# Optimization experiments

Measured on AMD Instinct MI355X. Metric: run time of the kernel, lower is better.

The kernel has to match this reference:

```python
import jax, jax.numpy as jnp
import numpy as np
from jax import lax

WIN = 9  # NCC window per axis (default [9]*3)

# 3x3x3 edge/shape kernels, shape [O=1, I=1, 3, 3, 3]
_LAP = np.zeros((3, 3, 3), np.float32)
_LAP[1, 1, 1] = 6.0
_LAP[0, 1, 1] = _LAP[2, 1, 1] = -1.0
_LAP[1, 0, 1] = _LAP[1, 2, 1] = -1.0
_LAP[1, 1, 0] = _LAP[1, 1, 2] = -1.0
LAP_K = jnp.asarray(_LAP)[None, None]

_row = np.array([[-1.0, 0.0, 1.0], [-2.0, 0.0, 2.0], [-1.0, 0.0, 1.0]], np.float32)
SOBEL_X = jnp.asarray(np.stack([_row, _row, _row], axis=0))[None, None]
_plane = np.array([[-1.0, -2.0, -1.0], [-1.0, -2.0, -1.0], [-1.0, -2.0, -1.0]], np.float32)
SOBEL_Y = jnp.asarray(np.stack([_plane, np.zeros((3, 3), np.float32), -_plane], axis=0))[None, None]
_zp = np.array([[-1.0, -1.0, -1.0], [0.0, 0.0, 0.0], [1.0, 1.0, 1.0]], np.float32)
SOBEL_Z = jnp.asarray(np.stack([_zp, 2.0 * _zp, _zp], axis=0))[None, None]


def conv3d(x, k, pad):
    # x: [N,C,D,H,W], k: [O,I,kd,kh,kw]
    return lax.conv_general_dilated(x, k, (1, 1, 1), [(pad, pad)] * 3)


def box_sum(x, win=WIN):
    # Separable all-ones box filter == dense ones conv (same math, fewer FLOPs)
    pad = win // 2
    for axis in range(3):
        kshape = [1, 1, 1, 1, 1]
        kshape[2 + axis] = win
        k = jnp.ones(kshape, x.dtype)
        padding = [(pad, pad) if a == axis else (0, 0) for a in range(3)]
        x = lax.conv_general_dilated(x, k, (1, 1, 1), padding)
    return x


def ncc_vxm(Ii, Ji, win=WIN):
    win_size = float(win ** 3)
    I2, J2, IJ = Ii * Ii, Ji * Ji, Ii * Ji
    I_sum = box_sum(Ii, win)
    J_sum = box_sum(Ji, win)
    I2_sum = box_sum(I2, win)
    J2_sum = box_sum(J2, win)
    IJ_sum = box_sum(IJ, win)
    u_I = I_sum / win_size
    u_J = J_sum / win_size
    cross = IJ_sum - u_J * I_sum - u_I * J_sum + u_I * u_J * win_size
    I_var = I2_sum - 2.0 * u_I * I_sum + u_I * u_I * win_size
    J_var = J2_sum - 2.0 * u_J * J_sum + u_J * u_J * win_size
    cc = cross * cross / (I_var * J_var + 1e-5)
    return -jnp.mean(cc)


def edge_detection(v):
    return conv3d(v, LAP_K, pad=1)


def shape_detection(v):
    gx = conv3d(v, SOBEL_X, pad=1)
    gy = conv3d(v, SOBEL_Y, pad=1)
    gz = conv3d(v, SOBEL_Z, pad=1)
    return jnp.sqrt(gx * gx + gy * gy + gz * gz)


def setup_inputs() -> dict:
    key = jax.random.key(0)
    k1, k2 = jax.random.split(key)
    shape = (1, 1, 160, 192, 160)
    y_true = jax.random.uniform(k1, shape, dtype=jnp.float32)
    y_pred = jax.random.uniform(k2, shape, dtype=jnp.float32)
    return {"y_true": y_true, "y_pred": y_pred}


def reference(y_true, y_pred):
    loss_orig = ncc_vxm(y_true, y_pred)
    loss_edge = ncc_vxm(edge_detection(y_true), edge_detection(y_pred))
    loss_shape = ncc_vxm(shape_detection(y_true), shape_detection(y_pred))
    return 0.8 * loss_orig + 0.1 * loss_edge + 0.1 * loss_shape
```

## Files before the change

kernel.cpp:

```cpp
#include <hip/hip_runtime.h>
#include <hip/hip_fp16.h>
#include <math.h>

#define DD 160
#define HHH 192
#define WWW 160
constexpr int HW = HHH * WWW;
constexpr int NV = DD * HHH * WWW;
constexpr int W4 = WWW / 4;
constexpr int HC = 4;
constexpr int DC = 4;
constexpr int SC = 8;

constexpr int NB_WH  = (W4 * DD * (HHH / HC)) / 256;
constexpr int NB_SO  = (W4 * HHH * (DD / SC)) / 256;
constexpr int NB_LAP = (NV / 4) / 256;
constexpr int NB_DCC = (W4 * HHH * (DD / DC)) / 256;

__device__ __forceinline__ int xcd_swz(int b, int n) {
    int q = n >> 3;
    return (b & 7) * q + (b >> 3);
}

__device__ __forceinline__ float4 ldg4(const float* __restrict__ p, int idx, bool ok) {
    float4 z = make_float4(0.f, 0.f, 0.f, 0.f);
    return ok ? *(const float4*)(p + idx) : z;
}

__device__ __forceinline__ void st_h4(__half* __restrict__ t, int idx,
                                      float s0, float s1, float s2, float s3) {
    union { __half2 h2[2]; uint2 u; } pk;
    pk.h2[0] = __floats2half2_rn(s0, s1);
    pk.h2[1] = __floats2half2_rn(s2, s3);
    *(uint2*)(t + idx) = pk.u;
}

__device__ __forceinline__ void ld_h4(const __half* __restrict__ t, int idx, float o[4]) {
    union { __half2 h2[2]; uint2 u; } pk;
    pk.u = *(const uint2*)(t + idx);
    o[0] = __low2float(pk.h2[0]); o[1] = __high2float(pk.h2[0]);
    o[2] = __low2float(pk.h2[1]); o[3] = __high2float(pk.h2[1]);
}

__device__ __forceinline__ void lap_body(int t, const float* __restrict__ a,
                                         const float* __restrict__ b,
                                         __half* __restrict__ oa, __half* __restrict__ ob) {
    int w = (t % W4) * 4;
    int h = (t / W4) % HHH;
    int d = t / (W4 * HHH);
    int idx = (d * HHH + h) * WWW + w;
    bool dok0 = d > 0, dok1 = d < DD - 1, hok0 = h > 0, hok1 = h < HHH - 1;
#pragma unroll
    for (int s = 0; s < 2; s++) {
        const float* p = s ? b : a;
        __half* o = s ? ob : oa;
        float4 c = *(const float4*)(p + idx);
        float m1 = (w > 0) ? p[idx - 1] : 0.f;
        float p4 = (w + 4 < WWW) ? p[idx + 4] : 0.f;
        float4 dm = ldg4(p, idx - HW, dok0);
        float4 dp = ldg4(p, idx + HW, dok1);
        float4 hm = ldg4(p, idx - WWW, hok0);
        float4 hp = ldg4(p, idx + WWW, hok1);
        st_h4(o, idx,
              6.f * c.x - (m1 + c.y + dm.x + dp.x + hm.x + hp.x),
              6.f * c.y - (c.x + c.z + dm.y + dp.y + hm.y + hp.y),
              6.f * c.z - (c.y + c.w + dm.z + dp.z + hm.z + hp.z),
              6.f * c.w - (c.z + p4 + dm.w + dp.w + hm.w + hp.w));
    }
}

__device__ __forceinline__ void sobel_slice(const float* __restrict__ p, int s, int h, int w,
                                            float a1[4], float a2[4], float a3[4]) {
#pragma unroll
    for (int k = 0; k < 4; k++) { a1[k] = 0.f; a2[k] = 0.f; a3[k] = 0.f; }
#pragma unroll
    for (int kh = -1; kh <= 1; kh++) {
        int h2 = h + kh;
        if ((unsigned)h2 < (unsigned)HHH) {
            int rb = (s * HHH + h2) * WWW + w;
            float4 cen = *(const float4*)(p + rb);
            float xm = (w > 0) ? p[rb - 1] : 0.f;
            float xp = (w + 4 < WWW) ? p[rb + 4] : 0.f;
            float xv[6] = {xm, cen.x, cen.y, cen.z, cen.w, xp};
            float smh = (kh == 0) ? 2.f : 1.f;
            float grh = (float)kh;
#pragma unroll
            for (int k = 0; k < 4; k++) {
                float gw = xv[k + 2] - xv[k];
                float pw = xv[k] + xv[k + 1] + xv[k + 2];
                float sw = pw + xv[k + 1];
                a1[k] += smh * gw;
                a2[k] += sw;
                a3[k] += grh * pw;
            }
        }
    }
}

__device__ __forceinline__ void sobel_body(int t, const float* __restrict__ a,
                                           const float* __restrict__ b,
                                           __half* __restrict__ oa, __half* __restrict__ ob) {
    int w = (t % W4) * 4;
    int h = (t / W4) % HHH;
    int c = t / (W4 * HHH);
    int d0 = c * SC;

    float A1[2][3][4], A2[2][3][4], A3[2][3][4];
#pragma unroll
    for (int r = 0; r < 2; r++)
#pragma unroll
        for (int j = 0; j < 3; j++)
#pragma unroll
            for (int k = 0; k < 4; k++) { A1[r][j][k] = 0.f; A2[r][j][k] = 0.f; A3[r][j][k] = 0.f; }

#pragma unroll
    for (int i = 0; i < SC + 2; i++) {
        int s = d0 - 1 + i;
#pragma unroll
        for (int r = 0; r < 2; r++)
#pragma unroll
            for (int k = 0; k < 4; k++) {
                A1[r][0][k] = A1[r][1][k]; A2[r][0][k] = A2[r][1][k]; A3[r][0][k] = A3[r][1][k];
                A1[r][1][k] = A1[r][2][k]; A2[r][1][k] = A2[r][2][k]; A3[r][1][k] = A3[r][2][k];
            }
        if (s >= 0 && s < DD) {
            sobel_slice(a, s, h, w, A1[0][2], A2[0][2], A3[0][2]);
            sobel_slice(b, s, h, w, A1[1][2], A2[1][2], A3[1][2]);
        } else {
#pragma unroll
            for (int r = 0; r < 2; r++)
#pragma unroll
                for (int k = 0; k < 4; k++) { A1[r][2][k] = 0.f; A2[r][2][k] = 0.f; A3[r][2][k] = 0.f; }
        }
        if (i >= 2) {
            int d = s - 1;
            int idx = (d * HHH + h) * WWW + w;
            float va[4], vb[4];
#pragma unroll
            for (int k = 0; k < 4; k++) {
                float gx = A1[0][0][k] + A1[0][1][k] + A1[0][2][k];
                float gy = A2[0][2][k] - A2[0][0][k];
                float gz = A3[0][0][k] + 2.f * A3[0][1][k] + A3[0][2][k];
                va[k] = sqrtf(gx * gx + gy * gy + gz * gz);
                gx = A1[1][0][k] + A1[1][1][k] + A1[1][2][k];
                gy = A2[1][2][k] - A2[1][0][k];
                gz = A3[1][0][k] + 2.f * A3[1][1][k] + A3[1][2][k];
                vb[k] = sqrtf(gx * gx + gy * gy + gz * gz);
            }
            st_h4(oa, idx, va[0], va[1], va[2], va[3]);
            st_h4(ob, idx, vb[0], vb[1], vb[2], vb[3]);
        }
    }
}

__device__ __forceinline__ void q5_from(const float x[12], const float y[12], float q[5][4]) {
    float s0 = 0, s1 = 0, s2 = 0, s3 = 0, s4 = 0;
#pragma unroll
    for (int j = 0; j < 9; j++) {
        s0 += x[j]; s1 += y[j];
        s2 += x[j] * x[j]; s3 += y[j] * y[j]; s4 += x[j] * y[j];
    }
    q[0][0] = s0; q[1][0] = s1; q[2][0] = s2; q[3][0] = s3; q[4][0] = s4;
#pragma unroll
    for (int k = 1; k < 4; k++) {
        q[0][k] = q[0][k - 1] + x[k + 8] - x[k - 1];
        q[1][k] = q[1][k - 1] + y[k + 8] - y[k - 1];
        q[2][k] = q[2][k - 1] + x[k + 8] * x[k + 8] - x[k - 1] * x[k - 1];
        q[3][k] = q[3][k - 1] + y[k + 8] * y[k + 8] - y[k - 1] * y[k - 1];
        q[4][k] = q[4][k - 1] + x[k + 8] * y[k + 8] - x[k - 1] * y[k - 1];
    }
}

__device__ __forceinline__ void ld12(const float* __restrict__ p, int rowbase, int w, float x[12]) {
    bool lo = (w >= 4);
    bool hi = (w + 7 < WWW);
    float4 x0 = ldg4(p, rowbase + w - 4, lo);
    float4 x1 = *(const float4*)(p + rowbase + w);
    float4 x2 = ldg4(p, rowbase + w + 4, hi);
    x[0] = x0.x; x[1] = x0.y; x[2] = x0.z; x[3] = x0.w;
    x[4] = x1.x; x[5] = x1.y; x[6] = x1.z; x[7] = x1.w;
    x[8] = x2.x; x[9] = x2.y; x[10] = x2.z; x[11] = x2.w;
}

__device__ __forceinline__ void ld12(const __half* __restrict__ p, int rowbase, int w, float x[12]) {
    bool lo = (w >= 4);
    bool hi = (w + 7 < WWW);
    union { __half2 h2[2]; uint2 u; } u0, u1, u2;
    uint2 z = make_uint2(0, 0);
    u0.u = lo ? *(const uint2*)(p + rowbase + w - 4) : z;
    u1.u = *(const uint2*)(p + rowbase + w);
    u2.u = hi ? *(const uint2*)(p + rowbase + w + 4) : z;
    x[0] = __low2float(u0.h2[0]); x[1] = __high2float(u0.h2[0]);
    x[2] = __low2float(u0.h2[1]); x[3] = __high2float(u0.h2[1]);
    x[4] = __low2float(u1.h2[0]); x[5] = __high2float(u1.h2[0]);
    x[6] = __low2float(u1.h2[1]); x[7] = __high2float(u1.h2[1]);
    x[8] = __low2float(u2.h2[0]); x[9] = __high2float(u2.h2[0]);
    x[10] = __low2float(u2.h2[1]); x[11] = __high2float(u2.h2[1]);
}

template <typename T>
__device__ __forceinline__ void rowq5(const T* __restrict__ a, const T* __restrict__ b,
                                      int rowbase, int w, float q[5][4]) {
    float x[12], y[12];
    ld12(a, rowbase, w, x);
    ld12(b, rowbase, w, y);
    q5_from(x, y, q);
}

template <typename T>
__device__ void whsum_body(int t, const T* __restrict__ a, const T* __restrict__ b,
                           __half* __restrict__ t0, __half* __restrict__ t1,
                           __half* __restrict__ t2, __half* __restrict__ t3,
                           __half* __restrict__ t4) {
    int w = (t % W4) * 4;
    int d = (t / W4) % DD;
    int c = t / (W4 * DD);
    int h0 = c * HC;

    float S[5][4] = {{0}};
    for (int j = 0; j < 9; j++) {
        int r = h0 - 4 + j;
        if ((unsigned)r < (unsigned)HHH) {
            float q[5][4];
            rowq5(a, b, (d * HHH + r) * WWW, w, q);
#pragma unroll
            for (int qq = 0; qq < 5; qq++)
#pragma unroll
                for (int k = 0; k < 4; k++) S[qq][k] += q[qq][k];
        }
    }
    {
        int idx = (d * HHH + h0) * WWW + w;
        st_h4(t0, idx, S[0][0], S[0][1], S[0][2], S[0][3]);
        st_h4(t1, idx, S[1][0], S[1][1], S[1][2], S[1][3]);
        st_h4(t2, idx, S[2][0], S[2][1], S[2][2], S[2][3]);
        st_h4(t3, idx, S[3][0], S[3][1], S[3][2], S[3][3]);
        st_h4(t4, idx, S[4][0], S[4][1], S[4][2], S[4][3]);
    }
    for (int h = h0 + 1; h < h0 + HC; h++) {
        int rin = h + 4, rout = h - 5;
        if (rin < HHH) {
            float q[5][4];
            rowq5(a, b, (d * HHH + rin) * WWW, w, q);
#pragma unroll
            for (int qq = 0; qq < 5; qq++)
#pragma unroll
                for (int k = 0; k < 4; k++) S[qq][k] += q[qq][k];
        }
        if (rout >= 0) {
            float q[5][4];
            rowq5(a, b, (d * HHH + rout) * WWW, w, q);
#pragma unroll
            for (int qq = 0; qq < 5; qq++)
#pragma unroll
                for (int k = 0; k < 4; k++) S[qq][k] -= q[qq][k];
        }
        int idx = (d * HHH + h) * WWW + w;
        st_h4(t0, idx, S[0][0], S[0][1], S[0][2], S[0][3]);
        st_h4(t1, idx, S[1][0], S[1][1], S[1][2], S[1][3]);
        st_h4(t2, idx, S[2][0], S[2][1], S[2][2], S[2][3]);
        st_h4(t3, idx, S[3][0], S[3][1], S[3][2], S[3][3]);
        st_h4(t4, idx, S[4][0], S[4][1], S[4][2], S[4][3]);
    }
}

__device__ __forceinline__ float cc1(float s0, float s1, float s2, float s3, float s4) {
    const float wsz = 729.0f;
    const float inv = 1.0f / 729.0f;
    float uI = s0 * inv;
    float uJ = s1 * inv;
    float cross = s4 - uJ * s0 - uI * s1 + uI * uJ * wsz;
    float Iv = s2 - 2.0f * uI * s0 + uI * uI * wsz;
    float Jv = s3 - 2.0f * uJ * s1 + uJ * uJ * wsz;
    return cross * cross / (Iv * Jv + 1e-5f);
}

__device__ void dcc_body(int t, const __half* __restrict__ t0, const __half* __restrict__ t1,
                         const __half* __restrict__ t2, const __half* __restrict__ t3,
                         const __half* __restrict__ t4, double* __restrict__ acc, int pair) {
    int w = (t % W4) * 4;
    int h = (t / W4) % HHH;
    int c = t / (W4 * HHH);
    int d0 = c * DC;

    float S[5][4] = {{0}};
    for (int j = 0; j < 9; j++) {
        int r = d0 - 4 + j;
        if ((unsigned)r < (unsigned)DD) {
            int idx = (r * HHH + h) * WWW + w;
            float v[5][4];
            ld_h4(t0, idx, v[0]); ld_h4(t1, idx, v[1]); ld_h4(t2, idx, v[2]);
            ld_h4(t3, idx, v[3]); ld_h4(t4, idx, v[4]);
#pragma unroll
            for (int q = 0; q < 5; q++)
#pragma unroll
                for (int k = 0; k < 4; k++) S[q][k] += v[q][k];
        }
    }
    float local = 0.f;
#pragma unroll
    for (int k = 0; k < 4; k++) local += cc1(S[0][k], S[1][k], S[2][k], S[3][k], S[4][k]);
#pragma unroll
    for (int d = 1; d < DC; d++) {
        int rin = d0 + d + 4, rout = d0 + d - 5;
        if (rin < DD) {
            int idx = (rin * HHH + h) * WWW + w;
            float v[5][4];
            ld_h4(t0, idx, v[0]); ld_h4(t1, idx, v[1]); ld_h4(t2, idx, v[2]);
            ld_h4(t3, idx, v[3]); ld_h4(t4, idx, v[4]);
#pragma unroll
            for (int q = 0; q < 5; q++)
#pragma unroll
                for (int k = 0; k < 4; k++) S[q][k] += v[q][k];
        }
        if (rout >= 0) {
            int idx = (rout * HHH + h) * WWW + w;
            float v[5][4];
            ld_h4(t0, idx, v[0]); ld_h4(t1, idx, v[1]); ld_h4(t2, idx, v[2]);
            ld_h4(t3, idx, v[3]); ld_h4(t4, idx, v[4]);
#pragma unroll
            for (int q = 0; q < 5; q++)
#pragma unroll
                for (int k = 0; k < 4; k++) S[q][k] -= v[q][k];
        }
#pragma unroll
        for (int k = 0; k < 4; k++) local += cc1(S[0][k], S[1][k], S[2][k], S[3][k], S[4][k]);
    }

    for (int off = 32; off > 0; off >>= 1) local += __shfl_down(local, off);
    __shared__ float wsum_[4];
    if ((threadIdx.x & 63) == 0) wsum_[threadIdx.x >> 6] = local;
    __syncthreads();
    if (threadIdx.x == 0) {
        float s = wsum_[0] + wsum_[1] + wsum_[2] + wsum_[3];
        atomicAdd(&acc[pair], (double)s);
    }
}

__global__ void stage1(const float* __restrict__ yt, const float* __restrict__ yp,
                       __half* __restrict__ e1a, __half* __restrict__ e1b,
                       __half* __restrict__ e2a, __half* __restrict__ e2b,
                       __half* __restrict__ ta0, __half* __restrict__ ta1,
                       __half* __restrict__ ta2, __half* __restrict__ ta3,
                       __half* __restrict__ ta4, double* __restrict__ acc) {
    int b = blockIdx.x;
    if (b < NB_WH) {
        int lb = xcd_swz(b, NB_WH);
        whsum_body<float>(lb * 256 + threadIdx.x, yt, yp, ta0, ta1, ta2, ta3, ta4);
    } else if (b < NB_WH + NB_SO) {
        int lb = xcd_swz(b - NB_WH, NB_SO);
        sobel_body(lb * 256 + threadIdx.x, yt, yp, e2a, e2b);
    } else if (b < NB_WH + NB_SO + NB_LAP) {
        int lb = xcd_swz(b - NB_WH - NB_SO, NB_LAP);
        lap_body(lb * 256 + threadIdx.x, yt, yp, e1a, e1b);
    } else {
        if (threadIdx.x < 3) acc[threadIdx.x] = 0.0;
    }
}

__global__ void stage23(const __half* __restrict__ ea, const __half* __restrict__ eb,
                        __half* __restrict__ o0, __half* __restrict__ o1,
                        __half* __restrict__ o2, __half* __restrict__ o3,
                        __half* __restrict__ o4,
                        const __half* __restrict__ i0, const __half* __restrict__ i1,
                        const __half* __restrict__ i2, const __half* __restrict__ i3,
                        const __half* __restrict__ i4, double* __restrict__ acc, int pair) {
    int b = blockIdx.x;
    if (b < NB_WH) {
        int lb = xcd_swz(b, NB_WH);
        whsum_body<__half>(lb * 256 + threadIdx.x, ea, eb, o0, o1, o2, o3, o4);
    } else {
        int lb = xcd_swz(b - NB_WH, NB_DCC);
        dcc_body(lb * 256 + threadIdx.x, i0, i1, i2, i3, i4, acc, pair);
    }
}

__global__ void dcc_k(const __half* __restrict__ t0, const __half* __restrict__ t1,
                      const __half* __restrict__ t2, const __half* __restrict__ t3,
                      const __half* __restrict__ t4, double* __restrict__ acc, int pair) {
    int lb = xcd_swz(blockIdx.x, NB_DCC);
    dcc_body(lb * 256 + threadIdx.x, t0, t1, t2, t3, t4, acc, pair);
}

__global__ void stage2b(const __half* __restrict__ e1a, const __half* __restrict__ e1b,
                        const __half* __restrict__ e2a, const __half* __restrict__ e2b,
                        __half* __restrict__ tB, __half* __restrict__ tC,
                        const __half* __restrict__ tA, double* __restrict__ acc) {
    int b = blockIdx.x;
    size_t nv = (size_t)NV;
    if (b < NB_WH) {
        int lb = xcd_swz(b, NB_WH);
        whsum_body<__half>(lb * 256 + threadIdx.x, e1a, e1b,
                           tB, tB + nv, tB + 2 * nv, tB + 3 * nv, tB + 4 * nv);
    } else if (b < 2 * NB_WH) {
        int lb = xcd_swz(b - NB_WH, NB_WH);
        whsum_body<__half>(lb * 256 + threadIdx.x, e2a, e2b,
                           tC, tC + nv, tC + 2 * nv, tC + 3 * nv, tC + 4 * nv);
    } else {
        int lb = xcd_swz(b - 2 * NB_WH, NB_DCC);
        dcc_body(lb * 256 + threadIdx.x,
                 tA, tA + nv, tA + 2 * nv, tA + 3 * nv, tA + 4 * nv, acc, 0);
    }
}

__global__ void stage3b(const __half* __restrict__ tB, const __half* __restrict__ tC,
                        double* __restrict__ acc) {
    int b = blockIdx.x;
    size_t nv = (size_t)NV;
    if (b < NB_DCC) {
        int lb = xcd_swz(b, NB_DCC);
        dcc_body(lb * 256 + threadIdx.x,
                 tB, tB + nv, tB + 2 * nv, tB + 3 * nv, tB + 4 * nv, acc, 1);
    } else {
        int lb = xcd_swz(b - NB_DCC, NB_DCC);
        dcc_body(lb * 256 + threadIdx.x,
                 tC, tC + nv, tC + 2 * nv, tC + 3 * nv, tC + 4 * nv, acc, 2);
    }
}

__global__ void finalize_k(const double* __restrict__ acc, float* __restrict__ out) {
    if (threadIdx.x == 0) {
        double v = 0.8 * acc[0] + 0.1 * acc[1] + 0.1 * acc[2];
        out[0] = (float)(-v / (double)NV);
    }
}

extern "C" void kernel_launch(void* const* d_in, const int* in_sizes, int n_in,
                              void* d_out, int out_size, void* d_ws, size_t ws_size,
                              hipStream_t stream) {
    const float* yt = (const float*)d_in[0];
    const float* yp = (const float*)d_in[1];
    float* out = (float*)d_out;

    double* acc = (double*)d_ws;
    __half* base = (__half*)((char*)d_ws + 256);
    size_t nv = (size_t)NV;
    __half* e1a = base + 0 * nv;
    __half* e1b = base + 1 * nv;
    __half* e2a = base + 2 * nv;
    __half* e2b = base + 3 * nv;
    __half* tA = base + 4 * nv;
    __half* tB = base + 9 * nv;
    __half* tC = base + 14 * nv;

    bool wide = ws_size >= 256 + 19 * nv * sizeof(__half);

    dim3 blk(256);

    hipLaunchKernelGGL(stage1, dim3(NB_WH + NB_SO + NB_LAP + 1), blk, 0, stream,
                       yt, yp, e1a, e1b, e2a, e2b,
                       tA, tA + nv, tA + 2 * nv, tA + 3 * nv, tA + 4 * nv, acc);

    if (wide) {
        hipLaunchKernelGGL(stage2b, dim3(2 * NB_WH + NB_DCC), blk, 0, stream,
                           e1a, e1b, e2a, e2b, tB, tC, tA, acc);
        hipLaunchKernelGGL(stage3b, dim3(2 * NB_DCC), blk, 0, stream, tB, tC, acc);
    } else {
        hipLaunchKernelGGL(stage23, dim3(NB_WH + NB_DCC), blk, 0, stream,
                           e1a, e1b,
                           tB, tB + nv, tB + 2 * nv, tB + 3 * nv, tB + 4 * nv,
                           tA, tA + nv, tA + 2 * nv, tA + 3 * nv, tA + 4 * nv,
                           acc, 0);
        hipLaunchKernelGGL(stage23, dim3(NB_WH + NB_DCC), blk, 0, stream,
                           e2a, e2b,
                           tA, tA + nv, tA + 2 * nv, tA + 3 * nv, tA + 4 * nv,
                           tB, tB + nv, tB + 2 * nv, tB + 3 * nv, tB + 4 * nv,
                           acc, 1);
        hipLaunchKernelGGL(dcc_k, dim3(NB_DCC), blk, 0, stream,
                           tA, tA + nv, tA + 2 * nv, tA + 3 * nv, tA + 4 * nv, acc, 2);
    }

    hipLaunchKernelGGL(finalize_k, dim3(1), dim3(1), 0, stream, acc, out);
}
```

Baseline: 359.9 us.

## Fuse Laplacian and Sobel into one pass and regroup stages by type

Adds a fused kernel that computes the Laplacian and the Sobel magnitude together from a single sliding 3x3x3 read of each input volume. Each thread walks a chunk of depth slices, keeping partial plane sums in registers so neighbouring slices are reused. The stages are then regrouped: all three W/H box-sum passes run in one launch and all three depth-sum/NCC reductions run in the next, instead of mixing the first pair's NCC into stage 2. The aim is to cut redundant global reads of the inputs and balance work across launches, at the cost of higher register pressure in the fused kernel.

```diff
diff --git a/kernel.cpp b/kernel.cpp
--- a/kernel.cpp
+++ b/kernel.cpp
@@ -11,11 +11,13 @@
 constexpr int HC = 4;
 constexpr int DC = 4;
 constexpr int SC = 8;
+constexpr int SCF = 4;
 
 constexpr int NB_WH  = (W4 * DD * (HHH / HC)) / 256;
 constexpr int NB_SO  = (W4 * HHH * (DD / SC)) / 256;
 constexpr int NB_LAP = (NV / 4) / 256;
 constexpr int NB_DCC = (W4 * HHH * (DD / DC)) / 256;
+constexpr int NB_FU  = (W4 * HHH * (DD / SCF)) / 256;
 
 __device__ __forceinline__ int xcd_swz(int b, int n) {
     int q = n >> 3;
@@ -40,6 +42,91 @@
     pk.u = *(const uint2*)(t + idx);
     o[0] = __low2float(pk.h2[0]); o[1] = __high2float(pk.h2[0]);
     o[2] = __low2float(pk.h2[1]); o[3] = __high2float(pk.h2[1]);
+}
+
+__device__ void fused_body(int t, const float* __restrict__ p,
+                           __half* __restrict__ olap, __half* __restrict__ osob) {
+    int w = (t % W4) * 4;
+    int h = (t / W4) % HHH;
+    int c = t / (W4 * HHH);
+    int d0 = c * SCF;
+
+    float A1[3][4], A2[3][4], A3[3][4];
+    float P6[6], PP4[4], PH[4];
+#pragma unroll
+    for (int j = 0; j < 3; j++)
+#pragma unroll
+        for (int k = 0; k < 4; k++) { A1[j][k] = 0.f; A2[j][k] = 0.f; A3[j][k] = 0.f; }
+#pragma unroll
+    for (int k = 0; k < 6; k++) P6[k] = 0.f;
+#pragma unroll
+    for (int k = 0; k < 4; k++) { PP4[k] = 0.f; PH[k] = 0.f; }
+
+#pragma unroll
+    for (int i = 0; i < SCF + 2; i++) {
+        int s = d0 - 1 + i;
+#pragma unroll
+        for (int k = 0; k < 4; k++) {
+            A1[0][k] = A1[1][k]; A2[0][k] = A2[1][k]; A3[0][k] = A3[1][k];
+            A1[1][k] = A1[2][k]; A2[1][k] = A2[2][k]; A3[1][k] = A3[2][k];
+        }
+        float C6[6] = {0.f, 0.f, 0.f, 0.f, 0.f, 0.f};
+        float CH[4] = {0.f, 0.f, 0.f, 0.f};
+#pragma unroll
+        for (int k = 0; k < 4; k++) { A1[2][k] = 0.f; A2[2][k] = 0.f; A3[2][k] = 0.f; }
+        if (s >= 0 && s < DD) {
+#pragma unroll
+            for (int kh = -1; kh <= 1; kh++) {
+                int h2 = h + kh;
+                if ((unsigned)h2 < (unsigned)HHH) {
+                    int rb = (s * HHH + h2) * WWW + w;
+                    float4 cen = *(const float4*)(p + rb);
+                    float xm = (w > 0) ? p[rb - 1] : 0.f;
+                    float xp = (w + 4 < WWW) ? p[rb + 4] : 0.f;
+                    float xv[6] = {xm, cen.x, cen.y, cen.z, cen.w, xp};
+                    float smh = (kh == 0) ? 2.f : 1.f;
+                    float grh = (float)kh;
+#pragma unroll
+                    for (int k = 0; k < 4; k++) {
+                        float gw = xv[k + 2] - xv[k];
+                        float pw = xv[k] + xv[k + 1] + xv[k + 2];
+                        float sw = pw + xv[k + 1];
+                        A1[2][k] += smh * gw;
+                        A2[2][k] += sw;
+                        A3[2][k] += grh * pw;
+                    }
+                    if (kh == 0) {
+#pragma unroll
+                        for (int j = 0; j < 6; j++) C6[j] = xv[j];
+                    } else {
+#pragma unroll
+                        for (int k = 0; k < 4; k++) CH[k] += xv[k + 1];
+                    }
+                }
+            }
+        }
+        if (i >= 2) {
+            int d = s - 1;
+            int idx = (d * HHH + h) * WWW + w;
+            float vs[4], vl[4];
+#pragma unroll
+            for (int k = 0; k < 4; k++) {
+                float gx = A1[0][k] + A1[1][k] + A1[2][k];
+                float gy = A2[2][k] - A2[0][k];
+                float gz = A3[0][k] + 2.f * A3[1][k] + A3[2][k];
+                vs[k] = sqrtf(gx * gx + gy * gy + gz * gz);
+                vl[k] = 6.f * P6[k + 1] - (P6[k] + P6[k + 2] + PH[k] + PP4[k] + C6[k + 1]);
+            }
+            st_h4(osob, idx, vs[0], vs[1], vs[2], vs[3]);
+            st_h4(olap, idx, vl[0], vl[1], vl[2], vl[3]);
+        }
+#pragma unroll
+        for (int k = 0; k < 4; k++) PP4[k] = P6[k + 1];
+#pragma unroll
+        for (int j = 0; j < 6; j++) P6[j] = C6[j];
+#pragma unroll
+        for (int k = 0; k < 4; k++) PH[k] = CH[k];
+    }
 }
 
 __device__ __forceinline__ void lap_body(int t, const float* __restrict__ a,
@@ -334,6 +421,64 @@
     if (threadIdx.x == 0) {
         float s = wsum_[0] + wsum_[1] + wsum_[2] + wsum_[3];
         atomicAdd(&acc[pair], (double)s);
+    }
+}
+
+__global__ void __launch_bounds__(256, 4)
+stage1f(const float* __restrict__ yt, const float* __restrict__ yp,
+        __half* __restrict__ e1a, __half* __restrict__ e1b,
+        __half* __restrict__ e2a, __half* __restrict__ e2b,
+        double* __restrict__ acc) {
+    int b = blockIdx.x;
+    if (b < NB_FU) {
+        int lb = xcd_swz(b, NB_FU);
+        fused_body(lb * 256 + threadIdx.x, yt, e1a, e2a);
+    } else if (b < 2 * NB_FU) {
+        int lb = xcd_swz(b - NB_FU, NB_FU);
+        fused_body(lb * 256 + threadIdx.x, yp, e1b, e2b);
+    } else {
+        if (threadIdx.x < 3) acc[threadIdx.x] = 0.0;
+    }
+}
+
+__global__ void stage2w(const float* __restrict__ yt, const float* __restrict__ yp,
+                        const __half* __restrict__ e1a, const __half* __restrict__ e1b,
+                        const __half* __restrict__ e2a, const __half* __restrict__ e2b,
+                        __half* __restrict__ tA, __half* __restrict__ tB,
+                        __half* __restrict__ tC) {
+    int b = blockIdx.x;
+    size_t nv = (size_t)NV;
+    if (b < NB_WH) {
+        int lb = xcd_swz(b, NB_WH);
+        whsum_body<float>(lb * 256 + threadIdx.x, yt, yp,
+                          tA, tA + nv, tA + 2 * nv, tA + 3 * nv, tA + 4 * nv);
+    } else if (b < 2 * NB_WH) {
+        int lb = xcd_swz(b - NB_WH, NB_WH);
+        whsum_body<__half>(lb * 256 + threadIdx.x, e1a, e1b,
+                           tB, tB + nv, tB + 2 * nv, tB + 3 * nv, tB + 4 * nv);
+    } else {
+        int lb = xcd_swz(b - 2 * NB_WH, NB_WH);
+        whsum_body<__half>(lb * 256 + threadIdx.x, e2a, e2b,
+                           tC, tC + nv, tC + 2 * nv, tC + 3 * nv, tC + 4 * nv);
+    }
+}
+
+__global__ void stage3w(const __half* __restrict__ tA, const __half* __restrict__ tB,
+                        const __half* __restrict__ tC, double* __restrict__ acc) {
+    int b = blockIdx.x;
+    size_t nv = (size_t)NV;
+    if (b < NB_DCC) {
+        int lb = xcd_swz(b, NB_DCC);
+        dcc_body(lb * 256 + threadIdx.x,
+                 tA, tA + nv, tA + 2 * nv, tA + 3 * nv, tA + 4 * nv, acc, 0);
+    } else if (b < 2 * NB_DCC) {
+        int lb = xcd_swz(b - NB_DCC, NB_DCC);
+        dcc_body(lb * 256 + threadIdx.x,
+                 tB, tB + nv, tB + 2 * nv, tB + 3 * nv, tB + 4 * nv, acc, 1);
+    } else {
+        int lb = xcd_swz(b - 2 * NB_DCC, NB_DCC);
+        dcc_body(lb * 256 + threadIdx.x,
+                 tC, tC + nv, tC + 2 * nv, tC + 3 * nv, tC + 4 * nv, acc, 2);
     }
 }
 
@@ -382,42 +527,6 @@
     dcc_body(lb * 256 + threadIdx.x, t0, t1, t2, t3, t4, acc, pair);
 }
 
-__global__ void stage2b(const __half* __restrict__ e1a, const __half* __restrict__ e1b,
-                        const __half* __restrict__ e2a, const __half* __restrict__ e2b,
-                        __half* __restrict__ tB, __half* __restrict__ tC,
-                        const __half* __restrict__ tA, double* __restrict__ acc) {
-    int b = blockIdx.x;
-    size_t nv = (size_t)NV;
-    if (b < NB_WH) {
-        int lb = xcd_swz(b, NB_WH);
-        whsum_body<__half>(lb * 256 + threadIdx.x, e1a, e1b,
-                           tB, tB + nv, tB + 2 * nv, tB + 3 * nv, tB + 4 * nv);
-    } else if (b < 2 * NB_WH) {
-        int lb = xcd_swz(b - NB_WH, NB_WH);
-        whsum_body<__half>(lb * 256 + threadIdx.x, e2a, e2b,
-                           tC, tC + nv, tC + 2 * nv, tC + 3 * nv, tC + 4 * nv);
-    } else {
-        int lb = xcd_swz(b - 2 * NB_WH, NB_DCC);
-        dcc_body(lb * 256 + threadIdx.x,
-                 tA, tA + nv, tA + 2 * nv, tA + 3 * nv, tA + 4 * nv, acc, 0);
-    }
-}
-
-__global__ void stage3b(const __half* __restrict__ tB, const __half* __restrict__ tC,
-                        double* __restrict__ acc) {
-    int b = blockIdx.x;
-    size_t nv = (size_t)NV;
-    if (b < NB_DCC) {
-        int lb = xcd_swz(b, NB_DCC);
-        dcc_body(lb * 256 + threadIdx.x,
-                 tB, tB + nv, tB + 2 * nv, tB + 3 * nv, tB + 4 * nv, acc, 1);
-    } else {
-        int lb = xcd_swz(b - NB_DCC, NB_DCC);
-        dcc_body(lb * 256 + threadIdx.x,
-                 tC, tC + nv, tC + 2 * nv, tC + 3 * nv, tC + 4 * nv, acc, 2);
-    }
-}
-
 __global__ void finalize_k(const double* __restrict__ acc, float* __restrict__ out) {
     if (threadIdx.x == 0) {
         double v = 0.8 * acc[0] + 0.1 * acc[1] + 0.1 * acc[2];
@@ -447,15 +556,17 @@
 
     dim3 blk(256);
 
-    hipLaunchKernelGGL(stage1, dim3(NB_WH + NB_SO + NB_LAP + 1), blk, 0, stream,
-                       yt, yp, e1a, e1b, e2a, e2b,
-                       tA, tA + nv, tA + 2 * nv, tA + 3 * nv, tA + 4 * nv, acc);
-
     if (wide) {
-        hipLaunchKernelGGL(stage2b, dim3(2 * NB_WH + NB_DCC), blk, 0, stream,
-                           e1a, e1b, e2a, e2b, tB, tC, tA, acc);
-        hipLaunchKernelGGL(stage3b, dim3(2 * NB_DCC), blk, 0, stream, tB, tC, acc);
+        hipLaunchKernelGGL(stage1f, dim3(2 * NB_FU + 1), blk, 0, stream,
+                           yt, yp, e1a, e1b, e2a, e2b, acc);
+        hipLaunchKernelGGL(stage2w, dim3(3 * NB_WH), blk, 0, stream,
+                           yt, yp, e1a, e1b, e2a, e2b, tA, tB, tC);
+        hipLaunchKernelGGL(stage3w, dim3(3 * NB_DCC), blk, 0, stream,
+                           tA, tB, tC, acc);
     } else {
+        hipLaunchKernelGGL(stage1, dim3(NB_WH + NB_SO + NB_LAP + 1), blk, 0, stream,
+                           yt, yp, e1a, e1b, e2a, e2b,
+                           tA, tA + nv, tA + 2 * nv, tA + 3 * nv, tA + 4 * nv, acc);
         hipLaunchKernelGGL(stage23, dim3(NB_WH + NB_DCC), blk, 0, stream,
                            e1a, e1b,
                            tB, tB + nv, tB + 2 * nv, tB + 3 * nv, tB + 4 * nv,
```

Measured after the change: 344.9 us. -4.2%, faster.
